# Kernel optimization log

Hardware: AMD Instinct MI355X
Metric: run time of the kernel (lower is better)

Reference implementation:

```python
import jax, jax.numpy as jnp
import numpy as np
import math

N_HEADS = 16
DIM_MODEL = 1024
DIM_KQ = 64
DIM_V = 64
B, T = 2, 2048


def setup_inputs() -> dict:
    key = jax.random.key(0)
    ks = jax.random.split(key, 9)
    s = 1.0 / math.sqrt(DIM_MODEL)
    return {
        "x": jax.random.normal(ks[0], (B, T, DIM_MODEL), dtype=jnp.float32),
        "Wq": jax.random.normal(ks[1], (DIM_MODEL, N_HEADS * DIM_KQ), dtype=jnp.float32) * s,
        "bq": jnp.zeros((N_HEADS * DIM_KQ,), dtype=jnp.float32),
        "Wk": jax.random.normal(ks[2], (DIM_MODEL, N_HEADS * DIM_KQ), dtype=jnp.float32) * s,
        "bk": jnp.zeros((N_HEADS * DIM_KQ,), dtype=jnp.float32),
        "Wv": jax.random.normal(ks[3], (DIM_MODEL, N_HEADS * DIM_V), dtype=jnp.float32) * s,
        "bv": jnp.zeros((N_HEADS * DIM_V,), dtype=jnp.float32),
        "Wo": jax.random.normal(ks[4], (N_HEADS * DIM_V, DIM_MODEL), dtype=jnp.float32) * s,
        "bo": jnp.zeros((DIM_MODEL,), dtype=jnp.float32),
    }


def reference(x, Wq, bq, Wk, bk, Wv, bv, Wo, bo):
    b, t, _ = x.shape
    # projections, split into heads: [B, T, h, d]
    q = (x @ Wq + bq).reshape(b, t, N_HEADS, DIM_KQ)
    k = (x @ Wk + bk).reshape(b, t, N_HEADS, DIM_KQ)
    v = (x @ Wv + bv).reshape(b, t, N_HEADS, DIM_V)
    # NOTE: faithful to source einsum 'B Tq h d, B Tk h d -> B h Tk Tq'
    # scores[b, h, tk, tq] = q[b, tq] . k[b, tk]
    scores = jnp.einsum('bqhd,bkhd->bhkq', q, k)
    # softmax over the LAST axis (= query axis tq), as in the source
    attn = jax.nn.softmax(scores / math.sqrt(DIM_KQ), axis=-1)
    # source einsum 'B h Tk Tq, B Tq h dv -> B Tq h dv':
    # sums over Tk only -> out[b, tq, h, dv] = v[b, tq, h, dv] * sum_tk attn[b, h, tk, tq]
    colsum = attn.sum(axis=2)                      # [B, h, Tq]
    mixed = v * colsum.transpose(0, 2, 1)[..., None]  # [B, Tq, h, dv]
    out = mixed.reshape(b, t, N_HEADS * DIM_V) @ Wo + bo
    return out
```

## Files before the change

### kernel.cpp

```cpp
#include <hip/hip_runtime.h>
#include <hip/hip_bf16.h>
#include <stdint.h>

typedef __attribute__((ext_vector_type(4))) float f32x4;
typedef __attribute__((ext_vector_type(8))) __bf16 bf16x8;

#define AS1 __attribute__((address_space(1)))
#define AS3 __attribute__((address_space(3)))

#if __has_builtin(__builtin_amdgcn_exp2f)
#define EXP2(x) __builtin_amdgcn_exp2f(x)
#else
#define EXP2(x) exp2f(x)
#endif

__device__ __forceinline__ ushort f2bf(float f) {
  uint32_t u = __builtin_bit_cast(uint32_t, f);
  u += 0x7fffu + ((u >> 16) & 1u);
  return (ushort)(u >> 16);
}
__device__ __forceinline__ float bf2f(ushort h) {
  uint32_t u = ((uint32_t)h) << 16;
  return __builtin_bit_cast(float, u);
}

#define SCK 0.18033688011112042f

#define GLD(src, dst) \
  __builtin_amdgcn_global_load_lds((const AS1 uint32_t*)(src), (AS3 uint32_t*)(dst), 16, 0, 0)

#define BARRIER()                          \
  do {                                     \
    __builtin_amdgcn_sched_barrier(0);     \
    __builtin_amdgcn_s_barrier();          \
    __builtin_amdgcn_sched_barrier(0);     \
  } while (0)


__global__ void k_cvt_x(const float* __restrict__ x, ushort* __restrict__ xb, int n4) {
  int i = blockIdx.x * blockDim.x + threadIdx.x;
  if (i >= n4) return;
  float4 v = ((const float4*)x)[i];
  ushort4 o;
  o.x = f2bf(v.x); o.y = f2bf(v.y); o.z = f2bf(v.z); o.w = f2bf(v.w);
  ((ushort4*)xb)[i] = o;
}

__global__ void k_prep_w(const float* __restrict__ Wq, const float* __restrict__ Wk,
                         const float* __restrict__ Wv, const float* __restrict__ Wo,
                         ushort* __restrict__ Wt, ushort* __restrict__ Wot) {
  __shared__ float tile[32][33];
  int z = blockIdx.z;
  const float* src = (z == 0) ? Wq : (z == 1) ? Wk : (z == 2) ? Wv : Wo;
  ushort* dst = (z < 3) ? (Wt + (size_t)z * 1048576) : Wot;
  float scale = (z == 1) ? SCK : 1.0f;
  int k0 = blockIdx.y * 32, n0 = blockIdx.x * 32;
  int tx = threadIdx.x, ty = threadIdx.y;
#pragma unroll
  for (int i = 0; i < 4; i++)
    tile[ty + i * 8][tx] = src[(size_t)(k0 + ty + i * 8) * 1024 + n0 + tx];
  __syncthreads();
#pragma unroll
  for (int i = 0; i < 4; i++)
    dst[(size_t)(n0 + ty + i * 8) * 1024 + k0 + tx] = f2bf(tile[tx][ty + i * 8] * scale);
}

template <int MODE>
__global__ __launch_bounds__(256, 3) void k_gemm(const ushort* __restrict__ A,
                                                 const ushort* __restrict__ Bt,
                                                 void* __restrict__ Cv,
                                                 const float* __restrict__ b0,
                                                 const float* __restrict__ b1,
                                                 const float* __restrict__ b2,
                                                 int K, int ldc) {
  __shared__ ushort As[128 * 64];
  __shared__ ushort Bs[128 * 64];
  const int tid = threadIdx.x;
  const int lane = tid & 63;
  const int wid = tid >> 6;
  const int wr = wid >> 1, wc = wid & 1;
  const int l15 = lane & 15, l4 = lane >> 4;

  const int chunk = (int)gridDim.x >> 3;
  const int L = blockIdx.x;
  const int f = (L & 7) * chunk + (L >> 3);
  const int row0 = (f & 31) * 128;
  const int col0 = (f >> 5) * 128;
  const int T = K >> 6;

  const int rt = tid >> 3;
  const int cswz = ((tid & 7) ^ (rt & 7)) * 8;
  const ushort* Ap = A + (size_t)(row0 + rt) * K + cswz;
  const ushort* Bp = Bt + (size_t)(col0 + rt) * K + cswz;

  int aoff[4][2], boff[4][2];
#pragma unroll
  for (int m = 0; m < 4; m++) {
    int r = wr * 64 + m * 16 + l15;
#pragma unroll
    for (int ks = 0; ks < 2; ks++)
      aoff[m][ks] = r * 128 + (((ks * 4 + l4) ^ (r & 7)) << 4);
  }
#pragma unroll
  for (int n = 0; n < 4; n++) {
    int r = wc * 64 + n * 16 + l15;
#pragma unroll
    for (int ks = 0; ks < 2; ks++)
      boff[n][ks] = r * 128 + (((ks * 4 + l4) ^ (r & 7)) << 4);
  }

  f32x4 acc[4][4] = {};

  for (int t = 0; t < T; ++t) {
#pragma unroll
    for (int i = 0; i < 4; i++)
      GLD(Ap + (size_t)(32 * i) * K + t * 64, (char*)As + (i * 256 + tid) * 16);
#pragma unroll
    for (int i = 0; i < 4; i++)
      GLD(Bp + (size_t)(32 * i) * K + t * 64, (char*)Bs + (i * 256 + tid) * 16);
    asm volatile("s_waitcnt vmcnt(0)" ::: "memory");
    BARRIER();

    bf16x8 af[4][2], bf_[4][2];
#pragma unroll
    for (int m = 0; m < 4; m++)
#pragma unroll
      for (int ks = 0; ks < 2; ks++)
        af[m][ks] = *(const bf16x8*)((const char*)As + aoff[m][ks]);
#pragma unroll
    for (int n = 0; n < 4; n++)
#pragma unroll
      for (int ks = 0; ks < 2; ks++)
        bf_[n][ks] = *(const bf16x8*)((const char*)Bs + boff[n][ks]);

    __builtin_amdgcn_s_setprio(1);
#pragma unroll
    for (int m = 0; m < 4; m++)
#pragma unroll
      for (int n = 0; n < 4; n++)
#pragma unroll
        for (int ks = 0; ks < 2; ks++)
          acc[m][n] = __builtin_amdgcn_mfma_f32_16x16x32_bf16(af[m][ks], bf_[n][ks],
                                                              acc[m][n], 0, 0, 0);
    __builtin_amdgcn_s_setprio(0);
    BARRIER();
  }

#pragma unroll
  for (int m = 0; m < 4; m++)
#pragma unroll
    for (int n = 0; n < 4; n++) {
      int colg = col0 + wc * 64 + n * 16 + l15;
      float bias;
      if (MODE == 0) {
        bias = (colg < 1024) ? b0[colg]
                             : ((colg < 2048) ? b1[colg - 1024] * SCK : b2[colg - 2048]);
      } else {
        bias = b0[colg];
      }
#pragma unroll
      for (int j = 0; j < 4; j++) {
        int rowg = row0 + wr * 64 + m * 16 + l4 * 4 + j;
        float v = acc[m][n][j] + bias;
        if (MODE == 0)
          ((ushort*)Cv)[(size_t)rowg * ldc + colg] = f2bf(v);
        else
          ((float*)Cv)[(size_t)rowg * ldc + colg] = v;
      }
    }
}

__global__ __launch_bounds__(256, 2) void k_attn_z(const ushort* __restrict__ QKV,
                                                   float* __restrict__ Zpart) {
  const int bid = blockIdx.x;
  const int xcd = bid & 7, kk = bid >> 3;
  const int g = xcd * 8 + (kk >> 3);
  const int tkb = kk & 7;
  const int bh = g & 31, s = g >> 5;
  const int b = bh >> 4, h = bh & 15;
  const int tid = threadIdx.x, lane = tid & 63, w = tid >> 6;
  const int l15 = lane & 15, l4 = lane >> 4;
  const size_t rs = 3072;

  __shared__ ushort Ks[256 * 64];
  __shared__ ushort Qs[3][128 * 64];

  const ushort* Kbase = QKV + (size_t)(b * 2048 + tkb * 256) * rs + 1024 + h * 64;
  const ushort* Qbase = QKV + (size_t)(b * 2048 + s * 1024) * rs + h * 64;

  const int csl = ((tid & 7) ^ ((tid >> 3) & 7)) * 8;

#pragma unroll
  for (int i = 0; i < 8; i++) {
    int c = i * 256 + tid;
    GLD(Kbase + (size_t)(c >> 3) * rs + csl, (char*)Ks + c * 16);
  }
  const ushort* gq[4];
#pragma unroll
  for (int i = 0; i < 4; i++) {
    int c = i * 256 + tid;
    gq[i] = Qbase + (size_t)(c >> 3) * rs + csl;
    GLD(gq[i], (char*)Qs[0] + c * 16);
  }
#pragma unroll
  for (int i = 0; i < 4; i++) {
    int c = i * 256 + tid;
    GLD(gq[i] + 128 * rs, (char*)Qs[1] + c * 16);
  }
  asm volatile("s_waitcnt vmcnt(4)" ::: "memory");
  BARRIER();

  bf16x8 kf[4][2];
#pragma unroll
  for (int m = 0; m < 4; m++)
#pragma unroll
    for (int d = 0; d < 2; d++) {
      int r = w * 64 + m * 16 + l15;
      kf[m][d] = *(const bf16x8*)((const char*)Ks + r * 128 + (((d * 4 + l4) ^ (r & 7)) << 4));
    }

  float z[4][4] = {};
  const f32x4 zero4 = {0.f, 0.f, 0.f, 0.f};

  for (int t = 0; t < 8; ++t) {
    if (t + 2 < 8) {
      char* qd = (char*)Qs[(t + 2) % 3];
#pragma unroll
      for (int i = 0; i < 4; i++) {
        int c = i * 256 + tid;
        GLD(gq[i] + (size_t)(t + 2) * 128 * rs, qd + c * 16);
      }
    }
    const char* qb = (const char*)Qs[t % 3];
    f32x4 acc[4][8];
    __builtin_amdgcn_s_setprio(1);
#pragma unroll
    for (int d = 0; d < 2; d++)
#pragma unroll
      for (int n = 0; n < 8; n++) {
        int r = n * 16 + l15;
        bf16x8 qf = *(const bf16x8*)(qb + r * 128 + (((d * 4 + l4) ^ (r & 7)) << 4));
#pragma unroll
        for (int m = 0; m < 4; m++)
          acc[m][n] = __builtin_amdgcn_mfma_f32_16x16x32_bf16(
              kf[m][d], qf, d == 0 ? zero4 : acc[m][n], 0, 0, 0);
      }
    __builtin_amdgcn_s_setprio(0);
#pragma unroll
    for (int m = 0; m < 4; m++)
#pragma unroll
      for (int n = 0; n < 8; n++)
#pragma unroll
        for (int j = 0; j < 4; j++) z[m][j] += EXP2(acc[m][n][j]);
    if (t < 6) {
      asm volatile("s_waitcnt vmcnt(4)" ::: "memory");
      BARRIER();
    } else if (t == 6) {
      asm volatile("s_waitcnt vmcnt(0)" ::: "memory");
      BARRIER();
    }
  }

#pragma unroll
  for (int m = 0; m < 4; m++)
#pragma unroll
    for (int j = 0; j < 4; j++) {
      float v = z[m][j];
      v += __shfl_xor(v, 1, 64);
      v += __shfl_xor(v, 2, 64);
      v += __shfl_xor(v, 4, 64);
      v += __shfl_xor(v, 8, 64);
      if (l15 == 0)
        Zpart[(size_t)s * 65536 + bh * 2048 + tkb * 256 + w * 64 + m * 16 + l4 * 4 + j] = v;
    }
}

__global__ void k_rz(const float* __restrict__ Zpart, float* __restrict__ rrz) {
  int g = blockIdx.x * 256 + threadIdx.x;
  rrz[g] = 1.0f / (Zpart[g] + Zpart[65536 + g]);
}

__global__ __launch_bounds__(256, 2) void k_attn_cs(const ushort* __restrict__ QKV,
                                                    const float* __restrict__ rrz,
                                                    float* __restrict__ csPart) {
  const int bid = blockIdx.x;
  const int xcd = bid & 7, kk = bid >> 3;
  const int g = xcd * 8 + (kk >> 3);
  const int tqb = kk & 7;
  const int bh = g & 31, s = g >> 5;
  const int b = bh >> 4, h = bh & 15;
  const int tid = threadIdx.x, lane = tid & 63, w = tid >> 6;
  const int l15 = lane & 15, l4 = lane >> 4;
  const size_t rs = 3072;

  __shared__ ushort Qs[256 * 64];
  __shared__ ushort Ks[3][128 * 64];

  const ushort* Qbase = QKV + (size_t)(b * 2048 + tqb * 256) * rs + h * 64;
  const ushort* Kbase = QKV + (size_t)(b * 2048 + s * 1024) * rs + 1024 + h * 64;
  const float* rz0 = rrz + bh * 2048 + s * 1024;

  const int csl = ((tid & 7) ^ ((tid >> 3) & 7)) * 8;

#pragma unroll
  for (int i = 0; i < 8; i++) {
    int c = i * 256 + tid;
    GLD(Qbase + (size_t)(c >> 3) * rs + csl, (char*)Qs + c * 16);
  }
  const ushort* gk[4];
#pragma unroll
  for (int i = 0; i < 4; i++) {
    int c = i * 256 + tid;
    gk[i] = Kbase + (size_t)(c >> 3) * rs + csl;
    GLD(gk[i], (char*)Ks[0] + c * 16);
  }
#pragma unroll
  for (int i = 0; i < 4; i++) {
    int c = i * 256 + tid;
    GLD(gk[i] + 128 * rs, (char*)Ks[1] + c * 16);
  }
  asm volatile("s_waitcnt vmcnt(4)" ::: "memory");
  BARRIER();

  bf16x8 qf[4][2];
#pragma unroll
  for (int m = 0; m < 4; m++)
#pragma unroll
    for (int d = 0; d < 2; d++) {
      int r = w * 64 + m * 16 + l15;
      qf[m][d] = *(const bf16x8*)((const char*)Qs + r * 128 + (((d * 4 + l4) ^ (r & 7)) << 4));
    }

  float cs[4][4] = {};
  const f32x4 zero4 = {0.f, 0.f, 0.f, 0.f};

  for (int t = 0; t < 8; ++t) {
    float rz[8];
#pragma unroll
    for (int n = 0; n < 8; n++) rz[n] = rz0[t * 128 + n * 16 + l15];
    if (t + 2 < 8) {
      char* kd = (char*)Ks[(t + 2) % 3];
#pragma unroll
      for (int i = 0; i < 4; i++) {
        int c = i * 256 + tid;
        GLD(gk[i] + (size_t)(t + 2) * 128 * rs, kd + c * 16);
      }
    }
    const char* kb = (const char*)Ks[t % 3];
    f32x4 acc[4][8];
    __builtin_amdgcn_s_setprio(1);
#pragma unroll
    for (int d = 0; d < 2; d++)
#pragma unroll
      for (int n = 0; n < 8; n++) {
        int r = n * 16 + l15;
        bf16x8 kft = *(const bf16x8*)(kb + r * 128 + (((d * 4 + l4) ^ (r & 7)) << 4));
#pragma unroll
        for (int m = 0; m < 4; m++)
          acc[m][n] = __builtin_amdgcn_mfma_f32_16x16x32_bf16(
              qf[m][d], kft, d == 0 ? zero4 : acc[m][n], 0, 0, 0);
      }
    __builtin_amdgcn_s_setprio(0);
#pragma unroll
    for (int m = 0; m < 4; m++)
#pragma unroll
      for (int n = 0; n < 8; n++)
#pragma unroll
        for (int j = 0; j < 4; j++)
          cs[m][j] = fmaf(EXP2(acc[m][n][j]), rz[n], cs[m][j]);
    if (t < 6) {
      asm volatile("s_waitcnt vmcnt(4)" ::: "memory");
      BARRIER();
    } else if (t == 6) {
      asm volatile("s_waitcnt vmcnt(0)" ::: "memory");
      BARRIER();
    }
  }

#pragma unroll
  for (int m = 0; m < 4; m++)
#pragma unroll
    for (int j = 0; j < 4; j++) {
      float v = cs[m][j];
      v += __shfl_xor(v, 1, 64);
      v += __shfl_xor(v, 2, 64);
      v += __shfl_xor(v, 4, 64);
      v += __shfl_xor(v, 8, 64);
      if (l15 == 0)
        csPart[(size_t)s * 65536 + bh * 2048 + tqb * 256 + w * 64 + m * 16 + l4 * 4 + j] = v;
    }
}

__global__ void k_mixed(const ushort* __restrict__ QKV, const float* __restrict__ csPart,
                        ushort* __restrict__ mixed) {
  int i = blockIdx.x * 256 + threadIdx.x;
  int row = i >> 7;
  int col = (i & 127) * 8;
  int b = row >> 11, t = row & 2047, h = col >> 6;
  int g = ((b << 4) + h) * 2048 + t;
  float cs = csPart[g] + csPart[65536 + g];
  uint4 raw = *(const uint4*)(QKV + (size_t)row * 3072 + 2048 + col);
  const ushort* pv = (const ushort*)&raw;
  ushort o[8];
#pragma unroll
  for (int k = 0; k < 8; k++) o[k] = f2bf(bf2f(pv[k]) * cs);
  *(uint4*)(mixed + (size_t)row * 1024 + col) = *(uint4*)o;
}


extern "C" void kernel_launch(void* const* d_in, const int* in_sizes, int n_in,
                              void* d_out, int out_size, void* d_ws, size_t ws_size,
                              hipStream_t stream) {
  const float* x = (const float*)d_in[0];
  const float* Wq = (const float*)d_in[1];
  const float* bq = (const float*)d_in[2];
  const float* Wk = (const float*)d_in[3];
  const float* bk = (const float*)d_in[4];
  const float* Wv = (const float*)d_in[5];
  const float* bv = (const float*)d_in[6];
  const float* Wo = (const float*)d_in[7];
  const float* bo = (const float*)d_in[8];

  char* ws = (char*)d_ws;
  ushort* xb     = (ushort*)(ws);
  ushort* Wt     = (ushort*)(ws + 8388608);
  ushort* Wot    = (ushort*)(ws + 14680064);
  ushort* QKV    = (ushort*)(ws + 16777216);
  float* Zpart   = (float*)(ws + 41943040);
  float* rrz     = (float*)(ws + 42467328);
  float* csPart  = (float*)(ws + 42729472);
  ushort* mixed  = (ushort*)(ws + 43253760);

  k_cvt_x<<<4096, 256, 0, stream>>>(x, xb, 4096 * 1024 / 4);
  k_prep_w<<<dim3(32, 32, 4), dim3(32, 8), 0, stream>>>(Wq, Wk, Wv, Wo, Wt, Wot);

  k_gemm<0><<<768, 256, 0, stream>>>(xb, Wt, QKV, bq, bk, bv, 1024, 3072);
  k_attn_z<<<512, 256, 0, stream>>>(QKV, Zpart);
  k_rz<<<256, 256, 0, stream>>>(Zpart, rrz);
  k_attn_cs<<<512, 256, 0, stream>>>(QKV, rrz, csPart);
  k_mixed<<<2048, 256, 0, stream>>>(QKV, csPart, mixed);
  k_gemm<1><<<256, 256, 0, stream>>>(mixed, Wot, d_out, bo, nullptr, nullptr, 1024, 1024);
}
```

Measured before the change: 124.1 us.

## Fuse prep kernels, fold rz into attn_cs, fuse colsum scaling into out GEMM

Merges the x conversion into the weight-prep launch and computes 1/Z inline in the colsum kernel, removing the k_rz kernel. The per-row colsum scaling of V is folded into a new output GEMM that reads V from QKV, scales it in registers, and writes it to LDS, so the separate mixed kernel and its intermediate buffer go away. The output GEMM now uses 128x64 tiles with 512 blocks and double buffering. This cuts three launches and one full intermediate round-trip. The cost is register-staged A loads with a full vmcnt(0) wait each iteration, which may expose latency in the out GEMM.

```diff
diff --git a/kernel.cpp b/kernel.cpp
--- a/kernel.cpp
+++ b/kernel.cpp
@@ -37,25 +37,29 @@
   } while (0)
 
 
-__global__ void k_cvt_x(const float* __restrict__ x, ushort* __restrict__ xb, int n4) {
-  int i = blockIdx.x * blockDim.x + threadIdx.x;
-  if (i >= n4) return;
-  float4 v = ((const float4*)x)[i];
-  ushort4 o;
-  o.x = f2bf(v.x); o.y = f2bf(v.y); o.z = f2bf(v.z); o.w = f2bf(v.w);
-  ((ushort4*)xb)[i] = o;
-}
-
-__global__ void k_prep_w(const float* __restrict__ Wq, const float* __restrict__ Wk,
-                         const float* __restrict__ Wv, const float* __restrict__ Wo,
-                         ushort* __restrict__ Wt, ushort* __restrict__ Wot) {
+__global__ void k_prep(const float* __restrict__ x, const float* __restrict__ Wq,
+                       const float* __restrict__ Wk, const float* __restrict__ Wv,
+                       const float* __restrict__ Wo, ushort* __restrict__ xb,
+                       ushort* __restrict__ Wt, ushort* __restrict__ Wot) {
   __shared__ float tile[32][33];
   int z = blockIdx.z;
+  int tx = threadIdx.x, ty = threadIdx.y;
+  if (z == 4) {
+    int base = (blockIdx.y * 32 + blockIdx.x) * 256 + ty * 32 + tx;
+#pragma unroll
+    for (int i = 0; i < 4; i++) {
+      int idx = base + i * 262144;
+      float4 v = ((const float4*)x)[idx];
+      ushort4 o;
+      o.x = f2bf(v.x); o.y = f2bf(v.y); o.z = f2bf(v.z); o.w = f2bf(v.w);
+      ((ushort4*)xb)[idx] = o;
+    }
+    return;
+  }
   const float* src = (z == 0) ? Wq : (z == 1) ? Wk : (z == 2) ? Wv : Wo;
   ushort* dst = (z < 3) ? (Wt + (size_t)z * 1048576) : Wot;
   float scale = (z == 1) ? SCK : 1.0f;
   int k0 = blockIdx.y * 32, n0 = blockIdx.x * 32;
-  int tx = threadIdx.x, ty = threadIdx.y;
 #pragma unroll
   for (int i = 0; i < 4; i++)
     tile[ty + i * 8][tx] = src[(size_t)(k0 + ty + i * 8) * 1024 + n0 + tx];
@@ -65,16 +69,15 @@
     dst[(size_t)(n0 + ty + i * 8) * 1024 + k0 + tx] = f2bf(tile[tx][ty + i * 8] * scale);
 }
 
-template <int MODE>
-__global__ __launch_bounds__(256, 3) void k_gemm(const ushort* __restrict__ A,
-                                                 const ushort* __restrict__ Bt,
-                                                 void* __restrict__ Cv,
-                                                 const float* __restrict__ b0,
-                                                 const float* __restrict__ b1,
-                                                 const float* __restrict__ b2,
-                                                 int K, int ldc) {
+__global__ __launch_bounds__(256, 3) void k_gemm_qkv(const ushort* __restrict__ A,
+                                                     const ushort* __restrict__ Bt,
+                                                     ushort* __restrict__ C,
+                                                     const float* __restrict__ b0,
+                                                     const float* __restrict__ b1,
+                                                     const float* __restrict__ b2) {
   __shared__ ushort As[128 * 64];
   __shared__ ushort Bs[128 * 64];
+  const int K = 1024, ldc = 3072;
   const int tid = threadIdx.x;
   const int lane = tid & 63;
   const int wid = tid >> 6;
@@ -151,21 +154,146 @@
 #pragma unroll
     for (int n = 0; n < 4; n++) {
       int colg = col0 + wc * 64 + n * 16 + l15;
-      float bias;
-      if (MODE == 0) {
-        bias = (colg < 1024) ? b0[colg]
-                             : ((colg < 2048) ? b1[colg - 1024] * SCK : b2[colg - 2048]);
-      } else {
-        bias = b0[colg];
-      }
+      float bias = (colg < 1024) ? b0[colg]
+                                 : ((colg < 2048) ? b1[colg - 1024] * SCK : b2[colg - 2048]);
 #pragma unroll
       for (int j = 0; j < 4; j++) {
         int rowg = row0 + wr * 64 + m * 16 + l4 * 4 + j;
-        float v = acc[m][n][j] + bias;
-        if (MODE == 0)
-          ((ushort*)Cv)[(size_t)rowg * ldc + colg] = f2bf(v);
-        else
-          ((float*)Cv)[(size_t)rowg * ldc + colg] = v;
+        C[(size_t)rowg * ldc + colg] = f2bf(acc[m][n][j] + bias);
+      }
+    }
+}
+
+__global__ __launch_bounds__(256, 2) void k_gemm_out(const ushort* __restrict__ QKV,
+                                                     const float* __restrict__ csPart,
+                                                     const ushort* __restrict__ Wot,
+                                                     float* __restrict__ out,
+                                                     const float* __restrict__ bo) {
+  __shared__ ushort As[2][128 * 64];
+  __shared__ ushort Bs[2][64 * 64];
+  const int tid = threadIdx.x;
+  const int lane = tid & 63;
+  const int wid = tid >> 6;
+  const int wr = wid >> 1, wc = wid & 1;
+  const int l15 = lane & 15, l4 = lane >> 4;
+
+  const int L = blockIdx.x;
+  const int f = (L & 7) * 64 + (L >> 3);
+  const int row0 = (f & 31) * 128;
+  const int col0 = (f >> 5) * 64;
+
+  const int rt = tid >> 3, sl = tid & 7;
+  int grow[4], gbh[4];
+#pragma unroll
+  for (int i = 0; i < 4; i++) {
+    grow[i] = row0 + 32 * i + rt;
+    gbh[i] = ((grow[i] >> 11) << 4) * 2048 + (grow[i] & 2047);
+  }
+
+  uint4 av[4];
+  float csv[4];
+
+#define ISSUE(t)                                                                   \
+  do {                                                                             \
+    _Pragma("unroll") for (int i = 0; i < 2; i++) {                                \
+      int c = i * 256 + tid;                                                       \
+      int rb = c >> 3;                                                             \
+      GLD(Wot + (size_t)(col0 + rb) * 1024 + (t) * 64 + (((c & 7) ^ (rb & 7)) * 8),\
+          (char*)Bs[(t) & 1] + c * 16);                                            \
+    }                                                                              \
+    _Pragma("unroll") for (int i = 0; i < 4; i++)                                  \
+        av[i] = *(const uint4*)(QKV + (size_t)grow[i] * 3072 + 2048 + (t) * 64 +   \
+                                sl * 8);                                           \
+    _Pragma("unroll") for (int i = 0; i < 4; i++) {                                \
+      int g = gbh[i] + (t) * 2048;                                                 \
+      csv[i] = csPart[g] + csPart[65536 + g];                                      \
+    }                                                                              \
+  } while (0)
+
+#define WRITE_A(t)                                                                 \
+  do {                                                                             \
+    _Pragma("unroll") for (int i = 0; i < 4; i++) {                                \
+      int r = 32 * i + rt;                                                         \
+      const ushort* pv = (const ushort*)&av[i];                                    \
+      ushort o[8];                                                                 \
+      _Pragma("unroll") for (int k = 0; k < 8; k++)                                \
+          o[k] = f2bf(bf2f(pv[k]) * csv[i]);                                       \
+      *(uint4*)((char*)As[(t) & 1] + r * 128 + ((sl ^ (r & 7)) << 4)) =            \
+          *(const uint4*)o;                                                        \
+    }                                                                              \
+  } while (0)
+
+  int aoff[4][2], boff[2][2];
+#pragma unroll
+  for (int m = 0; m < 4; m++) {
+    int r = wr * 64 + m * 16 + l15;
+#pragma unroll
+    for (int ks = 0; ks < 2; ks++)
+      aoff[m][ks] = r * 128 + (((ks * 4 + l4) ^ (r & 7)) << 4);
+  }
+#pragma unroll
+  for (int n = 0; n < 2; n++) {
+    int r = wc * 32 + n * 16 + l15;
+#pragma unroll
+    for (int ks = 0; ks < 2; ks++)
+      boff[n][ks] = r * 128 + (((ks * 4 + l4) ^ (r & 7)) << 4);
+  }
+
+  f32x4 acc[4][2] = {};
+
+  ISSUE(0);
+  asm volatile("s_waitcnt vmcnt(0)" ::: "memory");
+  WRITE_A(0);
+  asm volatile("s_waitcnt lgkmcnt(0)" ::: "memory");
+  BARRIER();
+
+  for (int t = 0; t < 16; ++t) {
+    if (t < 15) ISSUE(t + 1);
+    __builtin_amdgcn_sched_barrier(0);
+    const char* Ab = (const char*)As[t & 1];
+    const char* Bb = (const char*)Bs[t & 1];
+    bf16x8 af[4][2], bf_[2][2];
+#pragma unroll
+    for (int m = 0; m < 4; m++)
+#pragma unroll
+      for (int ks = 0; ks < 2; ks++)
+        af[m][ks] = *(const bf16x8*)(Ab + aoff[m][ks]);
+#pragma unroll
+    for (int n = 0; n < 2; n++)
+#pragma unroll
+      for (int ks = 0; ks < 2; ks++)
+        bf_[n][ks] = *(const bf16x8*)(Bb + boff[n][ks]);
+    __builtin_amdgcn_s_setprio(1);
+#pragma unroll
+    for (int m = 0; m < 4; m++)
+#pragma unroll
+      for (int n = 0; n < 2; n++)
+#pragma unroll
+        for (int ks = 0; ks < 2; ks++)
+          acc[m][n] = __builtin_amdgcn_mfma_f32_16x16x32_bf16(af[m][ks], bf_[n][ks],
+                                                              acc[m][n], 0, 0, 0);
+    __builtin_amdgcn_s_setprio(0);
+    if (t < 15) {
+      asm volatile("s_waitcnt vmcnt(0)" ::: "memory");
+      WRITE_A(t + 1);
+      asm volatile("s_waitcnt lgkmcnt(0)" ::: "memory");
+    }
+    BARRIER();
+  }
+
+#undef ISSUE
+#undef WRITE_A
+
+#pragma unroll
+  for (int m = 0; m < 4; m++)
+#pragma unroll
+    for (int n = 0; n < 2; n++) {
+      int colg = col0 + wc * 32 + n * 16 + l15;
+      float bias = bo[colg];
+#pragma unroll
+      for (int j = 0; j < 4; j++) {
+        int rowg = row0 + wr * 64 + m * 16 + l4 * 4 + j;
+        out[(size_t)rowg * 1024 + colg] = acc[m][n][j] + bias;
       }
     }
 }
@@ -275,13 +403,8 @@
     }
 }
 
-__global__ void k_rz(const float* __restrict__ Zpart, float* __restrict__ rrz) {
-  int g = blockIdx.x * 256 + threadIdx.x;
-  rrz[g] = 1.0f / (Zpart[g] + Zpart[65536 + g]);
-}
-
 __global__ __launch_bounds__(256, 2) void k_attn_cs(const ushort* __restrict__ QKV,
-                                                    const float* __restrict__ rrz,
+                                                    const float* __restrict__ Zpart,
                                                     float* __restrict__ csPart) {
   const int bid = blockIdx.x;
   const int xcd = bid & 7, kk = bid >> 3;
@@ -298,7 +421,7 @@
 
   const ushort* Qbase = QKV + (size_t)(b * 2048 + tqb * 256) * rs + h * 64;
   const ushort* Kbase = QKV + (size_t)(b * 2048 + s * 1024) * rs + 1024 + h * 64;
-  const float* rz0 = rrz + bh * 2048 + s * 1024;
+  const float* zp = Zpart + bh * 2048 + s * 1024;
 
   const int csl = ((tid & 7) ^ ((tid >> 3) & 7)) * 8;
 
@@ -337,7 +460,10 @@
   for (int t = 0; t < 8; ++t) {
     float rz[8];
 #pragma unroll
-    for (int n = 0; n < 8; n++) rz[n] = rz0[t * 128 + n * 16 + l15];
+    for (int n = 0; n < 8; n++) {
+      int idx = t * 128 + n * 16 + l15;
+      rz[n] = 1.0f / (zp[idx] + zp[65536 + idx]);
+    }
     if (t + 2 < 8) {
       char* kd = (char*)Ks[(t + 2) % 3];
 #pragma unroll
@@ -389,22 +515,6 @@
       if (l15 == 0)
         csPart[(size_t)s * 65536 + bh * 2048 + tqb * 256 + w * 64 + m * 16 + l4 * 4 + j] = v;
     }
-}
-
-__global__ void k_mixed(const ushort* __restrict__ QKV, const float* __restrict__ csPart,
-                        ushort* __restrict__ mixed) {
-  int i = blockIdx.x * 256 + threadIdx.x;
-  int row = i >> 7;
-  int col = (i & 127) * 8;
-  int b = row >> 11, t = row & 2047, h = col >> 6;
-  int g = ((b << 4) + h) * 2048 + t;
-  float cs = csPart[g] + csPart[65536 + g];
-  uint4 raw = *(const uint4*)(QKV + (size_t)row * 3072 + 2048 + col);
-  const ushort* pv = (const ushort*)&raw;
-  ushort o[8];
-#pragma unroll
-  for (int k = 0; k < 8; k++) o[k] = f2bf(bf2f(pv[k]) * cs);
-  *(uint4*)(mixed + (size_t)row * 1024 + col) = *(uint4*)o;
 }
 
 
@@ -427,17 +537,11 @@
   ushort* Wot    = (ushort*)(ws + 14680064);
   ushort* QKV    = (ushort*)(ws + 16777216);
   float* Zpart   = (float*)(ws + 41943040);
-  float* rrz     = (float*)(ws + 42467328);
-  float* csPart  = (float*)(ws + 42729472);
-  ushort* mixed  = (ushort*)(ws + 43253760);
-
-  k_cvt_x<<<4096, 256, 0, stream>>>(x, xb, 4096 * 1024 / 4);
-  k_prep_w<<<dim3(32, 32, 4), dim3(32, 8), 0, stream>>>(Wq, Wk, Wv, Wo, Wt, Wot);
-
-  k_gemm<0><<<768, 256, 0, stream>>>(xb, Wt, QKV, bq, bk, bv, 1024, 3072);
+  float* csPart  = (float*)(ws + 42467328);
+
+  k_prep<<<dim3(32, 32, 5), dim3(32, 8), 0, stream>>>(x, Wq, Wk, Wv, Wo, xb, Wt, Wot);
+  k_gemm_qkv<<<768, 256, 0, stream>>>(xb, Wt, QKV, bq, bk, bv);
   k_attn_z<<<512, 256, 0, stream>>>(QKV, Zpart);
-  k_rz<<<256, 256, 0, stream>>>(Zpart, rrz);
-  k_attn_cs<<<512, 256, 0, stream>>>(QKV, rrz, csPart);
-  k_mixed<<<2048, 256, 0, stream>>>(QKV, csPart, mixed);
-  k_gemm<1><<<256, 256, 0, stream>>>(mixed, Wot, d_out, bo, nullptr, nullptr, 1024, 1024);
-}
+  k_attn_cs<<<512, 256, 0, stream>>>(QKV, Zpart, csPart);
+  k_gemm_out<<<512, 256, 0, stream>>>(QKV, csPart, Wot, (float*)d_out, bo);
+}
```

Result: faster. 121.5 us (-2.1%).
